# Kernel optimization log

Measured on AMD Instinct MI355X. Metric: run time of the kernel, lower is better.

## Reference

```python
import jax, jax.numpy as jnp
import numpy as np

N = 50000
E = 800000
DIN = 128
DH = [128, 128]
DOUT = 64


def setup_inputs() -> dict:
    key = jax.random.key(0)
    ks = jax.random.split(key, 12)

    def w(k, fan_in, fan_out):
        return jax.random.normal(k, (fan_in, fan_out), dtype=jnp.float32) / np.sqrt(fan_in)

    x = jax.random.normal(ks[0], (N, DIN), dtype=jnp.float32)
    edge_index = jax.random.randint(ks[1], (2, E), 0, N, dtype=jnp.int64)
    return {
        "x": x,
        "edge_index": edge_index,
        # SAGEConv layer 0: lin_l (aggregated neighbors, with bias), lin_r (root, no bias)
        "Wl0": w(ks[2], DIN, DH[0]), "Wr0": w(ks[3], DIN, DH[0]), "b0": jnp.zeros((DH[0],), jnp.float32),
        # SAGEConv layer 1
        "Wl1": w(ks[4], DH[0], DH[1]), "Wr1": w(ks[5], DH[0], DH[1]), "b1": jnp.zeros((DH[1],), jnp.float32),
        # final Linear
        "Wout": w(ks[6], DH[1], DOUT), "bout": jnp.zeros((DOUT,), jnp.float32),
    }


def sage_conv(h, src, dst, Wl, Wr, b):
    # mean-aggregate source features at destination nodes
    msg = h[src]                                                  # [E, d]
    agg = jax.ops.segment_sum(msg, dst, num_segments=N)           # [N, d]
    cnt = jax.ops.segment_sum(jnp.ones((src.shape[0],), h.dtype), dst, num_segments=N)
    agg = agg / jnp.maximum(cnt, 1.0)[:, None]
    return agg @ Wl + h @ Wr + b


def reference(x, edge_index, Wl0, Wr0, b0, Wl1, Wr1, b1, Wout, bout):
    src, dst = edge_index[0], edge_index[1]
    h = jax.nn.relu(sage_conv(x, src, dst, Wl0, Wr0, b0))
    # dropout: identity in eval mode
    h = jax.nn.relu(sage_conv(h, src, dst, Wl1, Wr1, b1))
    out = h @ Wout + bout                                         # [N, DOUT]
    return jax.nn.softmax(out, axis=1)
```

## Files before the change

kernel.cpp:

```cpp
#include <hip/hip_runtime.h>


#define CAP 64
#define NBK 256
#define EPB 2048
#define BCAP8 768

typedef __attribute__((ext_vector_type(8))) short bf16x8;
typedef __attribute__((ext_vector_type(4))) float f32x4;

__device__ __forceinline__ unsigned short bf16_rtne(float f) {
    unsigned u = __float_as_uint(f);
    u += 0x7FFFu + ((u >> 16) & 1u);
    return (unsigned short)(u >> 16);
}

__device__ __forceinline__ void pack_w_body(const float* __restrict__ Wl,
                                            const float* __restrict__ Wr,
                                            unsigned short* __restrict__ Wp, int i) {
    int j = i & 7;
    int l = (i >> 3) & 63;
    int ntile = (i >> 9) & 7;
    int kstep = i >> 12;
    int k = kstep * 32 + (l >> 4) * 8 + j;
    int n = ntile * 16 + (l & 15);
    float v = (k < 128) ? Wl[k * 128 + n] : Wr[(k - 128) * 128 + n];
    Wp[i] = bf16_rtne(v);
}

__global__ __launch_bounds__(256) void bucket_prep_kernel(
        const int* __restrict__ src, const int* __restrict__ dst,
        unsigned int* __restrict__ gtail, unsigned int* __restrict__ gbuf,
        int E, int aBlocks,
        const float* __restrict__ x, unsigned short* __restrict__ xb, int n4, int cvtBlocks,
        const float* __restrict__ Wl0, const float* __restrict__ Wr0,
        unsigned short* __restrict__ Wp1,
        const float* __restrict__ Wl1, const float* __restrict__ Wr1,
        unsigned short* __restrict__ Wp2,
        const float* __restrict__ Wout, unsigned short* __restrict__ Wpo) {
    int b = blockIdx.x;
    if (b < aBlocks) {
        __shared__ unsigned int hist[NBK];
        __shared__ unsigned int pref[NBK + 1];
        __shared__ int baseS[NBK];
        __shared__ unsigned int scat[EPB];
        __shared__ unsigned char scatb[EPB];
        int tid = (int)threadIdx.x;
        int xcd = b & 7;
        hist[tid] = 0u;
        __syncthreads();

        int e0 = b * EPB + tid * 8;
        int dd[8], ss[8], bb[8];
        unsigned rr[8];
        bool vld[8];
        if (e0 + 7 < E) {
            int4 d0 = *(const int4*)(dst + e0);
            int4 d1 = *(const int4*)(dst + e0 + 4);
            int4 s0 = *(const int4*)(src + e0);
            int4 s1 = *(const int4*)(src + e0 + 4);
            dd[0] = d0.x; dd[1] = d0.y; dd[2] = d0.z; dd[3] = d0.w;
            dd[4] = d1.x; dd[5] = d1.y; dd[6] = d1.z; dd[7] = d1.w;
            ss[0] = s0.x; ss[1] = s0.y; ss[2] = s0.z; ss[3] = s0.w;
            ss[4] = s1.x; ss[5] = s1.y; ss[6] = s1.z; ss[7] = s1.w;
#pragma unroll
            for (int u = 0; u < 8; ++u) vld[u] = true;
        } else {
#pragma unroll
            for (int u = 0; u < 8; ++u) {
                int e = e0 + u;
                vld[u] = (e < E);
                dd[u] = vld[u] ? dst[e] : 0;
                ss[u] = vld[u] ? src[e] : 0;
            }
        }
#pragma unroll
        for (int u = 0; u < 8; ++u) {
            bb[u] = dd[u] >> 8;
            rr[u] = vld[u] ? atomicAdd(&hist[bb[u]], 1u) : 0u;
        }
        __syncthreads();
        pref[tid + 1] = hist[tid];
        if (tid == 0) pref[0] = 0u;
        __syncthreads();
        for (int off = 1; off < NBK; off <<= 1) {
            unsigned add = (tid + 1 > off) ? pref[tid + 1 - off] : 0u;
            __syncthreads();
            pref[tid + 1] += add;
            __syncthreads();
        }
        {
            unsigned h = hist[tid];
            unsigned gb0 = (h != 0u) ? atomicAdd(&gtail[xcd * NBK + tid], h) : 0u;
            baseS[tid] = (int)((unsigned)(xcd * NBK + tid) * BCAP8 + gb0) - (int)pref[tid];
        }
        __syncthreads();
#pragma unroll
        for (int u = 0; u < 8; ++u) {
            if (vld[u]) {
                unsigned idx = pref[bb[u]] + rr[u];
                scat[idx] = ((unsigned)dd[u] << 16) | (unsigned)(ss[u] & 0xFFFF);
                scatb[idx] = (unsigned char)bb[u];
            }
        }
        __syncthreads();
        unsigned tot = pref[NBK];
        for (unsigned i = (unsigned)tid; i < tot; i += 256u) {
            int bk = (int)scatb[i];
            int gi = baseS[bk] + (int)i;
            unsigned segBase = (unsigned)(xcd * NBK + bk) * BCAP8;
            if ((unsigned)gi - segBase < BCAP8) gbuf[gi] = scat[i];
        }
    } else if (b < aBlocks + cvtBlocks) {
        int i = (b - aBlocks) * 256 + (int)threadIdx.x;
        if (i < n4) {
            float4 v = ((const float4*)x)[i];
            ushort4 o;
            o.x = bf16_rtne(v.x); o.y = bf16_rtne(v.y);
            o.z = bf16_rtne(v.z); o.w = bf16_rtne(v.w);
            ((ushort4*)xb)[i] = o;
        }
    } else if (b < aBlocks + cvtBlocks + 128) {
        pack_w_body(Wl0, Wr0, Wp1, (b - aBlocks - cvtBlocks) * 256 + (int)threadIdx.x);
    } else if (b < aBlocks + cvtBlocks + 256) {
        pack_w_body(Wl1, Wr1, Wp2, (b - aBlocks - cvtBlocks - 128) * 256 + (int)threadIdx.x);
    } else {
        int i = (b - aBlocks - cvtBlocks - 256) * 256 + (int)threadIdx.x;
        int j = i & 7;
        int l = (i >> 3) & 63;
        int nt = (i >> 9) & 3;
        int ks = i >> 11;
        int k = ks * 32 + (l >> 4) * 8 + j;
        int n = nt * 16 + (l & 15);
        Wpo[i] = bf16_rtne(Wout[k * 64 + n]);
    }
}

__global__ __launch_bounds__(256) void fill_csr_kernel(
        const unsigned int* __restrict__ gtail, const unsigned int* __restrict__ gbuf,
        int* __restrict__ cnt, unsigned short* __restrict__ csr, int N) {
    __shared__ unsigned int cntL[256];
    __shared__ unsigned short stage[256 * CAP];
    int b = blockIdx.x;
    int tid = (int)threadIdx.x;
    cntL[tid] = 0u;
    __syncthreads();
#pragma unroll 1
    for (int xcd = 0; xcd < 8; ++xcd) {
        unsigned nE = gtail[xcd * NBK + b];
        if (nE > BCAP8) nE = BCAP8;
        const unsigned int* g = gbuf + (size_t)(xcd * NBK + b) * BCAP8;
        for (unsigned i = (unsigned)tid; i < nE; i += 256u) {
            unsigned pk = g[i];
            int dl = (int)((pk >> 16) & 255u);
            unsigned p = atomicAdd(&cntL[dl], 1u);
            if (p < CAP) stage[dl * CAP + p] = (unsigned short)(pk & 0xFFFFu);
        }
    }
    __syncthreads();
    const uint4* s4 = (const uint4*)stage;
    uint4* g4 = (uint4*)(csr + (size_t)b * (256 * CAP));
    for (int i = tid; i < (256 * CAP) / 8; i += 256) g4[i] = s4[i];
    int node = b * 256 + tid;
    if (node < N) cnt[node] = (int)cntL[tid];
}

__global__ __launch_bounds__(256) void agg_bf16_kernel(
        const unsigned short* __restrict__ hb, const int* __restrict__ cnt,
        const unsigned short* __restrict__ csr, unsigned short* __restrict__ aggb, int N) {
    int t = blockIdx.x * blockDim.x + threadIdx.x;
    int node = t >> 5;
    int lane = t & 31;
    if (node >= N) return;
    int deg = min(cnt[node], CAP);
    int s0 = node * CAP;
    int s1 = s0 + deg;
    const uint2* h2 = (const uint2*)hb;
    float a0 = 0.f, a1 = 0.f, a2 = 0.f, a3 = 0.f;
    for (int base = 0; base < deg; base += 32) {
        int nc = min(32, deg - base);
        int e = min(s0 + base + lane, s1 - 1);
        int idx = csr[e];
        for (int j = 0; j < nc; j += 8) {
            uint2 v[8];
#pragma unroll
            for (int u = 0; u < 8; ++u) {
                int sidx = __shfl(idx, j + u, 32);
                v[u] = h2[(size_t)sidx * 32 + lane];
            }
#pragma unroll
            for (int u = 0; u < 8; ++u) {
                unsigned vx = (j + u < nc) ? v[u].x : 0u;
                unsigned vy = (j + u < nc) ? v[u].y : 0u;
                a0 += __uint_as_float(vx << 16);
                a1 += __uint_as_float(vx & 0xFFFF0000u);
                a2 += __uint_as_float(vy << 16);
                a3 += __uint_as_float(vy & 0xFFFF0000u);
            }
        }
    }
    float inv = 1.0f / (float)max(deg, 1);
    ushort4 o;
    o.x = bf16_rtne(a0 * inv); o.y = bf16_rtne(a1 * inv);
    o.z = bf16_rtne(a2 * inv); o.w = bf16_rtne(a3 * inv);
    ((ushort4*)aggb)[(size_t)node * 32 + lane] = o;
}

__device__ __forceinline__ void mfma_dual_gemm(
        const unsigned short* __restrict__ aggb, const unsigned short* __restrict__ rootb,
        const unsigned short* __restrict__ Wp, int rowc, int quad, int lane,
        f32x4 acc[8]) {
#pragma unroll
    for (int t = 0; t < 8; ++t) acc[t] = (f32x4){0.f, 0.f, 0.f, 0.f};
    for (int ks = 0; ks < 8; ++ks) {
        const unsigned short* Abase = (ks < 4) ? aggb : rootb;
        int kloc = (ks & 3) * 32 + quad * 8;
        bf16x8 a = *(const bf16x8*)(Abase + (size_t)rowc * 128 + kloc);
#pragma unroll
        for (int t = 0; t < 8; ++t) {
            bf16x8 bf = *(const bf16x8*)(Wp + ((size_t)(ks * 8 + t) * 64 + lane) * 8);
            acc[t] = __builtin_amdgcn_mfma_f32_16x16x32_bf16(a, bf, acc[t], 0, 0, 0);
        }
    }
}

__global__ __launch_bounds__(256) void mfma_layer1_kernel(
        const unsigned short* __restrict__ aggb, const unsigned short* __restrict__ rootb,
        const unsigned short* __restrict__ Wp, const float* __restrict__ b,
        unsigned short* __restrict__ houtb, int N) {
    int lane = threadIdx.x & 63;
    int wv = threadIdx.x >> 6;
    int m0 = blockIdx.x * 64 + wv * 16;
    int quad = lane >> 4;
    int rowc = min(m0 + (lane & 15), N - 1);
    f32x4 acc[8];
    mfma_dual_gemm(aggb, rootb, Wp, rowc, quad, lane, acc);
    int colb = lane & 15;
#pragma unroll
    for (int t = 0; t < 8; ++t) {
        int col = t * 16 + colb;
        float bias = b[col];
#pragma unroll
        for (int r = 0; r < 4; ++r) {
            int node = m0 + quad * 4 + r;
            if (node < N) {
                float v = fmaxf(acc[t][r] + bias, 0.f);
                houtb[(size_t)node * 128 + col] = bf16_rtne(v);
            }
        }
    }
}

__global__ __launch_bounds__(256) void mfma_layer2_out_kernel(
        const unsigned short* __restrict__ aggb, const unsigned short* __restrict__ rootb,
        const unsigned short* __restrict__ Wp, const float* __restrict__ b,
        const unsigned short* __restrict__ Wpo, const float* __restrict__ bout,
        float* __restrict__ out, int N) {
    __shared__ unsigned short sH[4][16 * 128];
    int lane = threadIdx.x & 63;
    int wv = threadIdx.x >> 6;
    int m0 = blockIdx.x * 64 + wv * 16;
    int quad = lane >> 4;
    int c = lane & 15;
    int rowc = min(m0 + c, N - 1);
    f32x4 acc[8];
    mfma_dual_gemm(aggb, rootb, Wp, rowc, quad, lane, acc);
#pragma unroll
    for (int t = 0; t < 8; ++t) {
        int col = t * 16 + c;
        float bias = b[col];
#pragma unroll
        for (int r = 0; r < 4; ++r) {
            sH[wv][(quad * 4 + r) * 128 + col] = bf16_rtne(fmaxf(acc[t][r] + bias, 0.f));
        }
    }
    __syncthreads();

    f32x4 acc2[4];
#pragma unroll
    for (int nt = 0; nt < 4; ++nt) acc2[nt] = (f32x4){0.f, 0.f, 0.f, 0.f};
#pragma unroll
    for (int ks = 0; ks < 4; ++ks) {
        bf16x8 a = *(const bf16x8*)&sH[wv][c * 128 + ks * 32 + quad * 8];
#pragma unroll
        for (int nt = 0; nt < 4; ++nt) {
            bf16x8 bf = *(const bf16x8*)(Wpo + ((size_t)(ks * 4 + nt) * 64 + lane) * 8);
            acc2[nt] = __builtin_amdgcn_mfma_f32_16x16x32_bf16(a, bf, acc2[nt], 0, 0, 0);
        }
    }

    float bo[4];
#pragma unroll
    for (int nt = 0; nt < 4; ++nt) bo[nt] = bout[nt * 16 + c];
#pragma unroll
    for (int r = 0; r < 4; ++r) {
        float v[4];
#pragma unroll
        for (int nt = 0; nt < 4; ++nt) v[nt] = acc2[nt][r] + bo[nt];
        float m = fmaxf(fmaxf(v[0], v[1]), fmaxf(v[2], v[3]));
#pragma unroll
        for (int ofs = 1; ofs < 16; ofs <<= 1) m = fmaxf(m, __shfl_xor(m, ofs, 64));
        float e[4];
        float s = 0.f;
#pragma unroll
        for (int nt = 0; nt < 4; ++nt) { e[nt] = __expf(v[nt] - m); s += e[nt]; }
#pragma unroll
        for (int ofs = 1; ofs < 16; ofs <<= 1) s += __shfl_xor(s, ofs, 64);
        float inv = 1.0f / s;
        int node = m0 + quad * 4 + r;
        if (node < N) {
#pragma unroll
            for (int nt = 0; nt < 4; ++nt)
                out[(size_t)node * 64 + nt * 16 + c] = e[nt] * inv;
        }
    }
}

extern "C" void kernel_launch(void* const* d_in, const int* in_sizes, int n_in,
                              void* d_out, int out_size, void* d_ws, size_t ws_size,
                              hipStream_t stream) {
    const float* x    = (const float*)d_in[0];
    const int*   ei   = (const int*)d_in[1];
    const float* Wl0  = (const float*)d_in[2];
    const float* Wr0  = (const float*)d_in[3];
    const float* b0   = (const float*)d_in[4];
    const float* Wl1  = (const float*)d_in[5];
    const float* Wr1  = (const float*)d_in[6];
    const float* b1   = (const float*)d_in[7];
    const float* Wout = (const float*)d_in[8];
    const float* bout = (const float*)d_in[9];

    int N = in_sizes[0] / 128;
    int E = in_sizes[1] / 2;
    const int* src = ei;
    const int* dst = ei + E;
    int nb = (N + 255) >> 8;

    char* p = (char*)d_ws;
    auto alloc = [&](size_t bytes) -> char* {
        char* r = p;
        p += (bytes + 255) & ~(size_t)255;
        return r;
    };
    unsigned int*   gtail = (unsigned int*)alloc((size_t)8 * NBK * 4);
    unsigned int*   gbuf  = (unsigned int*)alloc((size_t)8 * NBK * BCAP8 * 4);
    int*            cnt   = (int*)alloc((size_t)N * 4);
    unsigned short* csr   = (unsigned short*)alloc((size_t)nb * 256 * CAP * 2);
    unsigned short* xb    = (unsigned short*)alloc((size_t)N * 128 * 2);
    unsigned short* h0b   = (unsigned short*)alloc((size_t)N * 128 * 2);
    unsigned short* aggb  = (unsigned short*)alloc((size_t)N * 128 * 2);
    unsigned short* Wp1   = (unsigned short*)alloc((size_t)32768 * 2);
    unsigned short* Wp2   = (unsigned short*)alloc((size_t)32768 * 2);
    unsigned short* Wpo   = (unsigned short*)alloc((size_t)8192 * 2);

    hipMemsetAsync(gtail, 0, (size_t)8 * NBK * 4, stream);

    int n4 = N * 128 / 4;
    int cvtBlocks = (n4 + 255) / 256;
    int aBlocks = (E + EPB - 1) / EPB;
    bucket_prep_kernel<<<aBlocks + cvtBlocks + 256 + 32, 256, 0, stream>>>(
        src, dst, gtail, gbuf, E, aBlocks,
        x, xb, n4, cvtBlocks, Wl0, Wr0, Wp1, Wl1, Wr1, Wp2, Wout, Wpo);

    fill_csr_kernel<<<nb, 256, 0, stream>>>(gtail, gbuf, cnt, csr, N);

    int ab = (N * 32 + 255) / 256;
    int gb = (N + 63) / 64;

    agg_bf16_kernel<<<ab, 256, 0, stream>>>(xb, cnt, csr, aggb, N);
    mfma_layer1_kernel<<<gb, 256, 0, stream>>>(aggb, xb, Wp1, b0, h0b, N);
    agg_bf16_kernel<<<ab, 256, 0, stream>>>(h0b, cnt, csr, aggb, N);
    mfma_layer2_out_kernel<<<gb, 256, 0, stream>>>(aggb, h0b, Wp2, b1,
                                                   Wpo, bout, (float*)d_out, N);
}
```

Measured before the change: 198.0 us.

## Fuse neighbor mean-aggregation into MFMA layer kernels via per-wave LDS tiles

Removes the separate aggregation kernels and the global agg buffer. Each wave now gathers and averages its 16 rows into a padded LDS tile, then feeds that tile straight into the dual MFMA GEMM. Each node is handled by a 16-lane group with 16-byte loads, four nodes processed one after another. This saves the global write and re-read of the aggregate plus two launches, but the gather parallelism per wave drops (16 lanes per node, serial over 4 nodes), which may hurt latency hiding.

```diff
diff --git a/kernel.cpp b/kernel.cpp
--- a/kernel.cpp
+++ b/kernel.cpp
@@ -5,6 +5,7 @@
 #define NBK 256
 #define EPB 2048
 #define BCAP8 768
+#define ASTR 136
 
 typedef __attribute__((ext_vector_type(8))) short bf16x8;
 typedef __attribute__((ext_vector_type(4))) float f32x4;
@@ -13,6 +14,10 @@
     unsigned u = __float_as_uint(f);
     u += 0x7FFFu + ((u >> 16) & 1u);
     return (unsigned short)(u >> 16);
+}
+
+__device__ __forceinline__ unsigned pack2(float lo, float hi) {
+    return (unsigned)bf16_rtne(lo) | ((unsigned)bf16_rtne(hi) << 16);
 }
 
 __device__ __forceinline__ void pack_w_body(const float* __restrict__ Wl,
@@ -165,57 +170,72 @@
     if (node < N) cnt[node] = (int)cntL[tid];
 }
 
-__global__ __launch_bounds__(256) void agg_bf16_kernel(
+__device__ __forceinline__ void gather_mean_lds(
         const unsigned short* __restrict__ hb, const int* __restrict__ cnt,
-        const unsigned short* __restrict__ csr, unsigned short* __restrict__ aggb, int N) {
-    int t = blockIdx.x * blockDim.x + threadIdx.x;
-    int node = t >> 5;
-    int lane = t & 31;
-    if (node >= N) return;
-    int deg = min(cnt[node], CAP);
-    int s0 = node * CAP;
-    int s1 = s0 + deg;
-    const uint2* h2 = (const uint2*)hb;
-    float a0 = 0.f, a1 = 0.f, a2 = 0.f, a3 = 0.f;
-    for (int base = 0; base < deg; base += 32) {
-        int nc = min(32, deg - base);
-        int e = min(s0 + base + lane, s1 - 1);
-        int idx = csr[e];
-        for (int j = 0; j < nc; j += 8) {
-            uint2 v[8];
-#pragma unroll
-            for (int u = 0; u < 8; ++u) {
-                int sidx = __shfl(idx, j + u, 32);
-                v[u] = h2[(size_t)sidx * 32 + lane];
+        const unsigned short* __restrict__ csr, unsigned short* __restrict__ sAw,
+        int m0, int lane, int N) {
+    int qw = lane >> 4;
+    int ql = lane & 15;
+    const uint4* h4 = (const uint4*)hb;
+#pragma unroll 1
+    for (int i = 0; i < 4; ++i) {
+        int nl = qw * 4 + i;
+        int node = m0 + nl;
+        int deg = (node < N) ? min(cnt[node], CAP) : 0;
+        int s0 = node * CAP;
+        int s1 = s0 + deg;
+        float a[8];
+#pragma unroll
+        for (int u = 0; u < 8; ++u) a[u] = 0.f;
+        for (int base = 0; base < deg; base += 16) {
+            int nc = min(16, deg - base);
+            int e = min(s0 + base + ql, s1 - 1);
+            int idx = csr[e];
+            for (int j = 0; j < nc; j += 8) {
+                uint4 v[8];
+#pragma unroll
+                for (int u = 0; u < 8; ++u) {
+                    int sidx = __shfl(idx, j + u, 16);
+                    v[u] = h4[(size_t)sidx * 16 + ql];
+                }
+#pragma unroll
+                for (int u = 0; u < 8; ++u) {
+                    bool ok = (j + u < nc);
+                    unsigned w0 = ok ? v[u].x : 0u;
+                    unsigned w1 = ok ? v[u].y : 0u;
+                    unsigned w2 = ok ? v[u].z : 0u;
+                    unsigned w3 = ok ? v[u].w : 0u;
+                    a[0] += __uint_as_float(w0 << 16);
+                    a[1] += __uint_as_float(w0 & 0xFFFF0000u);
+                    a[2] += __uint_as_float(w1 << 16);
+                    a[3] += __uint_as_float(w1 & 0xFFFF0000u);
+                    a[4] += __uint_as_float(w2 << 16);
+                    a[5] += __uint_as_float(w2 & 0xFFFF0000u);
+                    a[6] += __uint_as_float(w3 << 16);
+                    a[7] += __uint_as_float(w3 & 0xFFFF0000u);
+                }
             }
-#pragma unroll
-            for (int u = 0; u < 8; ++u) {
-                unsigned vx = (j + u < nc) ? v[u].x : 0u;
-                unsigned vy = (j + u < nc) ? v[u].y : 0u;
-                a0 += __uint_as_float(vx << 16);
-                a1 += __uint_as_float(vx & 0xFFFF0000u);
-                a2 += __uint_as_float(vy << 16);
-                a3 += __uint_as_float(vy & 0xFFFF0000u);
-            }
-        }
-    }
-    float inv = 1.0f / (float)max(deg, 1);
-    ushort4 o;
-    o.x = bf16_rtne(a0 * inv); o.y = bf16_rtne(a1 * inv);
-    o.z = bf16_rtne(a2 * inv); o.w = bf16_rtne(a3 * inv);
-    ((ushort4*)aggb)[(size_t)node * 32 + lane] = o;
-}
-
-__device__ __forceinline__ void mfma_dual_gemm(
-        const unsigned short* __restrict__ aggb, const unsigned short* __restrict__ rootb,
-        const unsigned short* __restrict__ Wp, int rowc, int quad, int lane,
+        }
+        float inv = 1.0f / (float)max(deg, 1);
+        uint4 o;
+        o.x = pack2(a[0] * inv, a[1] * inv);
+        o.y = pack2(a[2] * inv, a[3] * inv);
+        o.z = pack2(a[4] * inv, a[5] * inv);
+        o.w = pack2(a[6] * inv, a[7] * inv);
+        *(uint4*)(sAw + nl * ASTR + ql * 8) = o;
+    }
+}
+
+__device__ __forceinline__ void mfma_dual_gemm_lds(
+        const unsigned short* __restrict__ sAw, const unsigned short* __restrict__ rootb,
+        const unsigned short* __restrict__ Wp, int rowc, int quad, int c, int lane,
         f32x4 acc[8]) {
 #pragma unroll
     for (int t = 0; t < 8; ++t) acc[t] = (f32x4){0.f, 0.f, 0.f, 0.f};
     for (int ks = 0; ks < 8; ++ks) {
-        const unsigned short* Abase = (ks < 4) ? aggb : rootb;
-        int kloc = (ks & 3) * 32 + quad * 8;
-        bf16x8 a = *(const bf16x8*)(Abase + (size_t)rowc * 128 + kloc);
+        bf16x8 a;
+        if (ks < 4) a = *(const bf16x8*)(sAw + c * ASTR + ks * 32 + quad * 8);
+        else        a = *(const bf16x8*)(rootb + (size_t)rowc * 128 + (ks & 3) * 32 + quad * 8);
 #pragma unroll
         for (int t = 0; t < 8; ++t) {
             bf16x8 bf = *(const bf16x8*)(Wp + ((size_t)(ks * 8 + t) * 64 + lane) * 8);
@@ -224,21 +244,23 @@
     }
 }
 
-__global__ __launch_bounds__(256) void mfma_layer1_kernel(
-        const unsigned short* __restrict__ aggb, const unsigned short* __restrict__ rootb,
-        const unsigned short* __restrict__ Wp, const float* __restrict__ b,
-        unsigned short* __restrict__ houtb, int N) {
+__global__ __launch_bounds__(256) void fused_l1_kernel(
+        const unsigned short* __restrict__ hb, const int* __restrict__ cnt,
+        const unsigned short* __restrict__ csr, const unsigned short* __restrict__ Wp,
+        const float* __restrict__ b, unsigned short* __restrict__ houtb, int N) {
+    __shared__ unsigned short sA[4][16 * ASTR];
     int lane = threadIdx.x & 63;
     int wv = threadIdx.x >> 6;
     int m0 = blockIdx.x * 64 + wv * 16;
+    gather_mean_lds(hb, cnt, csr, &sA[wv][0], m0, lane, N);
     int quad = lane >> 4;
-    int rowc = min(m0 + (lane & 15), N - 1);
+    int c = lane & 15;
+    int rowc = min(m0 + c, N - 1);
     f32x4 acc[8];
-    mfma_dual_gemm(aggb, rootb, Wp, rowc, quad, lane, acc);
-    int colb = lane & 15;
+    mfma_dual_gemm_lds(&sA[wv][0], hb, Wp, rowc, quad, c, lane, acc);
 #pragma unroll
     for (int t = 0; t < 8; ++t) {
-        int col = t * 16 + colb;
+        int col = t * 16 + c;
         float bias = b[col];
 #pragma unroll
         for (int r = 0; r < 4; ++r) {
@@ -251,37 +273,38 @@
     }
 }
 
-__global__ __launch_bounds__(256) void mfma_layer2_out_kernel(
-        const unsigned short* __restrict__ aggb, const unsigned short* __restrict__ rootb,
-        const unsigned short* __restrict__ Wp, const float* __restrict__ b,
+__global__ __launch_bounds__(256) void fused_l2_kernel(
+        const unsigned short* __restrict__ hb, const int* __restrict__ cnt,
+        const unsigned short* __restrict__ csr, const unsigned short* __restrict__ Wp,
+        const float* __restrict__ b,
         const unsigned short* __restrict__ Wpo, const float* __restrict__ bout,
         float* __restrict__ out, int N) {
-    __shared__ unsigned short sH[4][16 * 128];
+    __shared__ unsigned short sA[4][16 * ASTR];
     int lane = threadIdx.x & 63;
     int wv = threadIdx.x >> 6;
     int m0 = blockIdx.x * 64 + wv * 16;
+    gather_mean_lds(hb, cnt, csr, &sA[wv][0], m0, lane, N);
     int quad = lane >> 4;
     int c = lane & 15;
     int rowc = min(m0 + c, N - 1);
     f32x4 acc[8];
-    mfma_dual_gemm(aggb, rootb, Wp, rowc, quad, lane, acc);
+    mfma_dual_gemm_lds(&sA[wv][0], hb, Wp, rowc, quad, c, lane, acc);
 #pragma unroll
     for (int t = 0; t < 8; ++t) {
         int col = t * 16 + c;
         float bias = b[col];
 #pragma unroll
         for (int r = 0; r < 4; ++r) {
-            sH[wv][(quad * 4 + r) * 128 + col] = bf16_rtne(fmaxf(acc[t][r] + bias, 0.f));
-        }
-    }
-    __syncthreads();
+            sA[wv][(quad * 4 + r) * ASTR + col] = bf16_rtne(fmaxf(acc[t][r] + bias, 0.f));
+        }
+    }
 
     f32x4 acc2[4];
 #pragma unroll
     for (int nt = 0; nt < 4; ++nt) acc2[nt] = (f32x4){0.f, 0.f, 0.f, 0.f};
 #pragma unroll
     for (int ks = 0; ks < 4; ++ks) {
-        bf16x8 a = *(const bf16x8*)&sH[wv][c * 128 + ks * 32 + quad * 8];
+        bf16x8 a = *(const bf16x8*)&sA[wv][c * ASTR + ks * 32 + quad * 8];
 #pragma unroll
         for (int nt = 0; nt < 4; ++nt) {
             bf16x8 bf = *(const bf16x8*)(Wpo + ((size_t)(ks * 4 + nt) * 64 + lane) * 8);
@@ -348,7 +371,6 @@
     unsigned short* csr   = (unsigned short*)alloc((size_t)nb * 256 * CAP * 2);
     unsigned short* xb    = (unsigned short*)alloc((size_t)N * 128 * 2);
     unsigned short* h0b   = (unsigned short*)alloc((size_t)N * 128 * 2);
-    unsigned short* aggb  = (unsigned short*)alloc((size_t)N * 128 * 2);
     unsigned short* Wp1   = (unsigned short*)alloc((size_t)32768 * 2);
     unsigned short* Wp2   = (unsigned short*)alloc((size_t)32768 * 2);
     unsigned short* Wpo   = (unsigned short*)alloc((size_t)8192 * 2);
@@ -364,12 +386,8 @@
 
     fill_csr_kernel<<<nb, 256, 0, stream>>>(gtail, gbuf, cnt, csr, N);
 
-    int ab = (N * 32 + 255) / 256;
     int gb = (N + 63) / 64;
-
-    agg_bf16_kernel<<<ab, 256, 0, stream>>>(xb, cnt, csr, aggb, N);
-    mfma_layer1_kernel<<<gb, 256, 0, stream>>>(aggb, xb, Wp1, b0, h0b, N);
-    agg_bf16_kernel<<<ab, 256, 0, stream>>>(h0b, cnt, csr, aggb, N);
-    mfma_layer2_out_kernel<<<gb, 256, 0, stream>>>(aggb, h0b, Wp2, b1,
-                                                   Wpo, bout, (float*)d_out, N);
-}
+    fused_l1_kernel<<<gb, 256, 0, stream>>>(xb, cnt, csr, Wp1, b0, h0b, N);
+    fused_l2_kernel<<<gb, 256, 0, stream>>>(h0b, cnt, csr, Wp2, b1,
+                                            Wpo, bout, (float*)d_out, N);
+}
```

After: 186.6 us. 1.06x faster.
